# Optimization experiments

Measured on AMD Instinct MI355X. Metric: run time of the kernel, lower is better.

## Reference

```python
import jax, jax.numpy as jnp
import numpy as np

B, S, D_IN, D_EMB, H = 2, 2048, 1024, 1024, 16
HD = D_EMB // H  # projection_dim = 64


def setup_inputs() -> dict:
    key = jax.random.key(0)
    ks = jax.random.split(key, 9)
    s_in = 1.0 / np.sqrt(D_IN)
    s_emb = 1.0 / np.sqrt(D_EMB)
    return {
        "inputs": jax.random.normal(ks[0], (B, S, D_IN), dtype=jnp.float32),
        "Wq": jax.random.uniform(ks[1], (D_IN, D_EMB), jnp.float32, -s_in, s_in),
        "bq": jax.random.uniform(ks[2], (D_EMB,), jnp.float32, -s_in, s_in),
        "Wk": jax.random.uniform(ks[3], (D_IN, D_EMB), jnp.float32, -s_in, s_in),
        "bk": jax.random.uniform(ks[4], (D_EMB,), jnp.float32, -s_in, s_in),
        "Wv": jax.random.uniform(ks[5], (D_IN, D_EMB), jnp.float32, -s_in, s_in),
        "bv": jax.random.uniform(ks[6], (D_EMB,), jnp.float32, -s_in, s_in),
        "Wo": jax.random.uniform(ks[7], (D_EMB, D_EMB), jnp.float32, -s_emb, s_emb),
        "bo": jax.random.uniform(ks[8], (D_EMB,), jnp.float32, -s_emb, s_emb),
    }


def reference(inputs, Wq, bq, Wk, bk, Wv, bv, Wo, bo):
    b, s, _ = inputs.shape
    # QKV projections -> [b, h, s, hd]
    def split_heads(x):
        return x.reshape(b, s, H, HD).transpose(0, 2, 1, 3)
    q = split_heads(inputs @ Wq + bq)
    k = split_heads(inputs @ Wk + bk)
    v = split_heads(inputs @ Wv + bv)
    scale = 1.0 / jnp.sqrt(jnp.float32(HD))
    logits = jnp.einsum('bhqd,bhkd->bhqk', q, k) * scale
    attn = jax.nn.softmax(logits, axis=-1)
    ctx = jnp.einsum('bhqk,bhkd->bhqd', attn, v)  # [b,h,s,hd]
    concat = ctx.transpose(0, 2, 1, 3).reshape(b, s, D_EMB)
    return concat @ Wo + bo
```

## Files before the change

### kernel.cpp

```cpp
#include <hip/hip_runtime.h>
#include <stdint.h>

#define S_ 2048
#define H_ 16

typedef short s16x8 __attribute__((ext_vector_type(8)));
typedef float f32x4 __attribute__((ext_vector_type(4)));
typedef float f32x16 __attribute__((ext_vector_type(16)));

__device__ __forceinline__ ushort f2bf(float f) {
    union { float f; uint32_t u; } v; v.f = f;
    uint32_t r = v.u + 0x7fffu + ((v.u >> 16) & 1u);
    return (ushort)(r >> 16);
}
__device__ __forceinline__ uint32_t cvtpk(float a, float b) {
    uint32_t r;
    asm("v_cvt_pk_bf16_f32 %0, %1, %2" : "=v"(r) : "v"(a), "v"(b));
    return r;
}
__device__ __forceinline__ void plswap(uint32_t& a, uint32_t& b) {
    auto r = __builtin_amdgcn_permlane32_swap((int)a, (int)b, false, false);
    a = (uint32_t)r[0];
    b = (uint32_t)r[1];
}
__device__ __forceinline__ float xmax32(float x) {
    uint32_t a = __float_as_uint(x), b = a;
    plswap(a, b);
    return fmaxf(__uint_as_float(a), __uint_as_float(b));
}
__device__ __forceinline__ float xadd32(float x) {
    uint32_t a = __float_as_uint(x), b = a;
    plswap(a, b);
    return __uint_as_float(a) + __uint_as_float(b);
}
__device__ __forceinline__ float exp2_fast(float x) {
    float r;
    asm("v_exp_f32 %0, %1" : "=v"(r) : "v"(x));
    return r;
}

__device__ __forceinline__ void gld16(ushort* lds, const ushort* g) {
    auto* gp = reinterpret_cast<uint32_t __attribute__((address_space(1)))*>(
        reinterpret_cast<uintptr_t>(g));
    auto* lp = reinterpret_cast<uint32_t __attribute__((address_space(3)))*>(
        reinterpret_cast<uintptr_t>(lds));
    __builtin_amdgcn_global_load_lds(gp, lp, 16, 0, 0);
}

__global__ void cast_bf16(const float* __restrict__ src, ushort* __restrict__ dst) {
    size_t i = ((size_t)blockIdx.x * 256 + threadIdx.x) * 8;
    float4 x = *(const float4*)(src + i);
    float4 y = *(const float4*)(src + i + 4);
    s16x8 r;
    r[0] = (short)f2bf(x.x); r[1] = (short)f2bf(x.y);
    r[2] = (short)f2bf(x.z); r[3] = (short)f2bf(x.w);
    r[4] = (short)f2bf(y.x); r[5] = (short)f2bf(y.y);
    r[6] = (short)f2bf(y.z); r[7] = (short)f2bf(y.w);
    *(s16x8*)(dst + i) = r;
}

__global__ void transpose_k4(const float* __restrict__ s0, const float* __restrict__ s1,
                             const float* __restrict__ s2, const float* __restrict__ s3,
                             ushort* __restrict__ d0, ushort* __restrict__ d1,
                             ushort* __restrict__ d2, ushort* __restrict__ d3) {
    const int z = blockIdx.z;
    const float* src = (z == 0) ? s0 : (z == 1) ? s1 : (z == 2) ? s2 : s3;
    ushort* dst      = (z == 0) ? d0 : (z == 1) ? d1 : (z == 2) ? d2 : d3;
    __shared__ ushort t[32][33];
    int bx = blockIdx.x * 32, by = blockIdx.y * 32;
    int x = threadIdx.x;
    for (int y = threadIdx.y; y < 32; y += 8)
        t[y][x] = f2bf(src[(size_t)(by + y) * 1024 + bx + x]);
    __syncthreads();
    for (int y = threadIdx.y; y < 32; y += 8)
        dst[(size_t)(bx + y) * 1024 + by + x] = t[x][y];
}

__global__ void gemm_bt(const ushort* __restrict__ A,
                        const ushort* __restrict__ Bt0, const ushort* __restrict__ Bt1,
                        const ushort* __restrict__ Bt2,
                        const float* __restrict__ bi0, const float* __restrict__ bi1,
                        const float* __restrict__ bi2,
                        void* __restrict__ o0, void* __restrict__ o1,
                        void* __restrict__ o2,
                        int mode0) {
    const int z = blockIdx.z;
    const ushort* Bt  = (z == 0) ? Bt0 : (z == 1) ? Bt1 : Bt2;
    const float* bia  = (z == 0) ? bi0 : (z == 1) ? bi1 : bi2;
    void* out         = (z == 0) ? o0  : (z == 1) ? o1  : o2;
    const int mode = mode0 + z;

    __shared__ __align__(16) ushort SMEM[2][4096];
    ushort* Asm = &SMEM[0][0];
    ushort* Bsm = &SMEM[1][0];

    const int t = threadIdx.x;
    const int lane = t & 63, w = t >> 6;
    const int wm = w >> 1, wn = w & 1;
    const int quad = lane >> 4, l16 = lane & 15;
    const int m0 = blockIdx.y * 128, n0 = blockIdx.x * 128;
    const int K = 1024;

    const f32x4 FZ = {0.f, 0.f, 0.f, 0.f};
    f32x4 acc[4][4];
#pragma unroll
    for (int i = 0; i < 4; i++)
#pragma unroll
        for (int j = 0; j < 4; j++) acc[i][j] = FZ;

    const ushort* Ap = A  + (size_t)(m0 + (t >> 2)) * K + (t & 3) * 8;
    const ushort* Bp = Bt + (size_t)(n0 + (t >> 2)) * K + (t & 3) * 8;
    ushort* AsmW = Asm + w * 512;
    ushort* BsmW = Bsm + w * 512;

    for (int kt = 0; kt < K / 32; ++kt) {
        __syncthreads();
        gld16(AsmW,        Ap + kt * 32);
        gld16(AsmW + 2048, Ap + (size_t)64 * K + kt * 32);
        gld16(BsmW,        Bp + kt * 32);
        gld16(BsmW + 2048, Bp + (size_t)64 * K + kt * 32);
        __syncthreads();

        s16x8 a[4], b[4];
#pragma unroll
        for (int i = 0; i < 4; i++) {
            int row = wm * 64 + i * 16 + l16;
            a[i] = *(const s16x8*)((const char*)Asm + row * 64 + quad * 16);
        }
#pragma unroll
        for (int j = 0; j < 4; j++) {
            int row = wn * 64 + j * 16 + l16;
            b[j] = *(const s16x8*)((const char*)Bsm + row * 64 + quad * 16);
        }
#pragma unroll
        for (int i = 0; i < 4; i++)
#pragma unroll
            for (int j = 0; j < 4; j++)
                acc[i][j] = __builtin_amdgcn_mfma_f32_16x16x32_bf16(a[i], b[j], acc[i][j], 0, 0, 0);
    }

    if (mode == 3) {
        ushort* T = Asm;
        const int b_ = m0 >> 11;
        const int s_base = m0 & 2047;
        __syncthreads();
#pragma unroll
        for (int half = 0; half < 2; ++half) {
            if (wn == half) {
#pragma unroll
                for (int j = 0; j < 4; j++) {
                    int nl = j * 16 + l16;
                    float bv = bia[n0 + half * 64 + nl];
#pragma unroll
                    for (int i = 0; i < 4; i++) {
#pragma unroll
                        for (int r = 0; r < 4; r++) {
                            int ml = wm * 64 + i * 16 + quad * 4 + r;
                            T[nl * 128 + (ml ^ ((nl & 15) << 3))] = f2bf(acc[i][j][r] + bv);
                        }
                    }
                }
            }
            __syncthreads();
            {
                int row = t >> 2, cg = (t & 3) * 32;
                int ng = n0 + half * 64 + row;
                int h = ng >> 6, d = ng & 63;
                ushort* op = (ushort*)out + ((size_t)((b_ * 16 + h) * 64 + d)) * 2048 + s_base + cg;
#pragma unroll
                for (int c = 0; c < 4; c++) {
                    int col = (cg + c * 8) ^ ((row & 15) << 3);
                    *(s16x8*)(op + c * 8) = *(const s16x8*)(T + row * 128 + col);
                }
            }
            __syncthreads();
        }
        return;
    }

#pragma unroll
    for (int j = 0; j < 4; j++) {
        int n = n0 + wn * 64 + j * 16 + l16;
        float bv = bia[n];
#pragma unroll
        for (int i = 0; i < 4; i++) {
#pragma unroll
            for (int r = 0; r < 4; r++) {
                int m = m0 + wm * 64 + i * 16 + quad * 4 + r;
                float v = acc[i][j][r] + bv;
                if (mode == 0) {
                    ((float*)out)[(size_t)m * 1024 + n] = v;
                } else {
                    int b_ = m >> 11, s = m & 2047;
                    int h = n >> 6, d = n & 63;
                    if (mode == 1)
                        ((ushort*)out)[((size_t)(b_ * 16 + h) * 2048 + s) * 64 + d] = f2bf(v * 0.18033688011112042f);
                    else
                        ((ushort*)out)[((size_t)(b_ * 16 + h) * 2048 + s) * 64 + d] = f2bf(v);
                }
            }
        }
    }
}

#define MFMA32(a, b, c) __builtin_amdgcn_mfma_f32_32x32x16_bf16(a, b, c, 0, 0, 0)

__global__ __launch_bounds__(256, 2) void attn(const ushort* __restrict__ q_ws,
                                               const ushort* __restrict__ k_ws,
                                               const ushort* __restrict__ vt_ws,
                                               ushort* __restrict__ ctx) {
    __shared__ __align__(16) ushort Kb[2][4096];
    __shared__ __align__(16) ushort Vb[2][4096];
    __shared__ ushort obuf[4][32][72];

    const int t = threadIdx.x, lane = t & 63, w = t >> 6;
    const int l32 = lane & 31, hi = lane >> 5;

    const int bid = blockIdx.x;
    const int j_ = bid >> 3;
    const int bh = (bid & 7) + 8 * (j_ >> 4);
    const int q0 = (j_ & 15) * 128 + w * 32;

    const ushort* Qg = q_ws + (size_t)bh * S_ * 64;
    const ushort* Kg = k_ws + (size_t)bh * S_ * 64;
    const ushort* Vg = vt_ws + (size_t)bh * 64 * S_;

    s16x8 qf[4];
#pragma unroll
    for (int dc = 0; dc < 4; dc++)
        qf[dc] = *(const s16x8*)&Qg[(size_t)(q0 + l32) * 64 + dc * 16 + hi * 8];

    const int sr = t >> 3;
    const int sc = (t & 7) ^ (sr & 7);
    const ushort* kS = Kg + sr * 64 + sc * 8;
    const ushort* vS = Vg + (size_t)sr * 2048 + sc * 8;
    ushort* ldsK0 = &Kb[0][w * 512];
    ushort* ldsV0 = &Vb[0][w * 512];
    ushort* ldsK1 = &Kb[1][w * 512];
    ushort* ldsV1 = &Vb[1][w * 512];

    int fo[4];
#pragma unroll
    for (int c = 0; c < 4; c++)
        fo[c] = l32 * 64 + ((((c << 1) | hi) ^ (l32 & 7)) << 3);

    const f32x16 Z16 = {0.f,0.f,0.f,0.f,0.f,0.f,0.f,0.f,0.f,0.f,0.f,0.f,0.f,0.f,0.f,0.f};
    f32x16 o0 = Z16, o1 = Z16;
    float m_run = -1e30f, l_run = 0.f;

    gld16(ldsK0,        kS);
    gld16(ldsK0 + 2048, kS + 2048);
    gld16(ldsV0,        vS);
    gld16(ldsV0 + 2048, vS + (size_t)32 * 2048);
    __syncthreads();

    for (int kt = 0; kt < S_ / 64; ++kt) {
        const int cur = kt & 1;
        if (kt != S_ / 64 - 1) {
            const ushort* kn = kS + (kt + 1) * 4096;
            const ushort* vn = vS + (kt + 1) * 64;
            ushort* dK = cur ? ldsK0 : ldsK1;
            ushort* dV = cur ? ldsV0 : ldsV1;
            gld16(dK,        kn);
            gld16(dK + 2048, kn + 2048);
            gld16(dV,        vn);
            gld16(dV + 2048, vn + (size_t)32 * 2048);
        }
        const ushort* KB = &Kb[cur][0];
        const ushort* VB = &Vb[cur][0];

        f32x16 s0 = Z16, s1 = Z16;
#pragma unroll
        for (int dc = 0; dc < 4; dc++) {
            s16x8 k0 = *(const s16x8*)(KB + fo[dc]);
            s16x8 k1 = *(const s16x8*)(KB + 2048 + fo[dc]);
            s0 = MFMA32(k0, qf[dc], s0);
            s1 = MFMA32(k1, qf[dc], s1);
        }

        float m0 = fmaxf(s0[0], s1[0]), m1 = fmaxf(s0[1], s1[1]);
        float m2 = fmaxf(s0[2], s1[2]), m3 = fmaxf(s0[3], s1[3]);
#pragma unroll
        for (int r = 4; r < 16; r += 4) {
            m0 = fmaxf(m0, fmaxf(s0[r],     s1[r]));
            m1 = fmaxf(m1, fmaxf(s0[r + 1], s1[r + 1]));
            m2 = fmaxf(m2, fmaxf(s0[r + 2], s1[r + 2]));
            m3 = fmaxf(m3, fmaxf(s0[r + 3], s1[r + 3]));
        }
        float mx = fmaxf(fmaxf(m0, m1), fmaxf(m2, m3));
        mx = xmax32(mx);
        float mnew = fmaxf(m_run, mx);
        float alpha = exp2_fast(m_run - mnew);
        m_run = mnew;

        float ra = 0.f, rb = 0.f;
#pragma unroll
        for (int r = 0; r < 16; r++) {
            s0[r] = exp2_fast(s0[r] - mnew); ra += s0[r];
            s1[r] = exp2_fast(s1[r] - mnew); rb += s1[r];
        }
        l_run = l_run * alpha + xadd32(ra + rb);

#pragma unroll
        for (int r = 0; r < 16; r++) { o0[r] *= alpha; o1[r] *= alpha; }

#pragma unroll
        for (int ks = 0; ks < 2; ks++) {
            const f32x16& p = ks ? s1 : s0;
            uint32_t u0 = cvtpk(p[0], p[1]),   u2 = cvtpk(p[4], p[5]);
            plswap(u0, u2);
            uint32_t u1 = cvtpk(p[2], p[3]),   u3 = cvtpk(p[6], p[7]);
            plswap(u1, u3);
            uint32_t w0 = cvtpk(p[8], p[9]),   w2 = cvtpk(p[12], p[13]);
            plswap(w0, w2);
            uint32_t w1 = cvtpk(p[10], p[11]), w3 = cvtpk(p[14], p[15]);
            plswap(w1, w3);
            union { uint32_t u[4]; s16x8 h; } F0, F1;
            F0.u[0] = u0; F0.u[1] = u1; F0.u[2] = u2; F0.u[3] = u3;
            F1.u[0] = w0; F1.u[1] = w1; F1.u[2] = w2; F1.u[3] = w3;

            const int kc0 = ks * 2, kc1 = ks * 2 + 1;
            s16x8 v00 = *(const s16x8*)(VB + fo[kc0]);
            s16x8 v01 = *(const s16x8*)(VB + 2048 + fo[kc0]);
            s16x8 v10 = *(const s16x8*)(VB + fo[kc1]);
            s16x8 v11 = *(const s16x8*)(VB + 2048 + fo[kc1]);
            o0 = MFMA32(v00, F0.h, o0); o1 = MFMA32(v01, F0.h, o1);
            o0 = MFMA32(v10, F1.h, o0); o1 = MFMA32(v11, F1.h, o1);
        }

        __syncthreads();
    }

    float inv = 1.0f / l_run;
#pragma unroll
    for (int r = 0; r < 16; r++) {
        int d0 = (r & 3) + 8 * (r >> 2) + 4 * hi;
        obuf[w][l32][d0]      = f2bf(o0[r] * inv);
        obuf[w][l32][32 + d0] = f2bf(o1[r] * inv);
    }
    asm volatile("s_waitcnt lgkmcnt(0)" ::: "memory");
    __builtin_amdgcn_sched_barrier(0);
    int b_ = bh >> 4, h = bh & 15;
    ushort* gp = ctx + ((size_t)(b_ * 2048 + q0 + l32)) * 1024 + h * 64 + hi * 32;
#pragma unroll
    for (int c = 0; c < 4; c++)
        *(s16x8*)(gp + c * 8) = *(const s16x8*)&obuf[w][l32][hi * 32 + c * 8];
}

extern "C" void kernel_launch(void* const* d_in, const int* in_sizes, int n_in,
                              void* d_out, int out_size, void* d_ws, size_t ws_size,
                              hipStream_t stream) {
    const float* X  = (const float*)d_in[0];
    const float* Wq = (const float*)d_in[1];
    const float* bq = (const float*)d_in[2];
    const float* Wk = (const float*)d_in[3];
    const float* bk = (const float*)d_in[4];
    const float* Wv = (const float*)d_in[5];
    const float* bv = (const float*)d_in[6];
    const float* Wo = (const float*)d_in[7];
    const float* bo = (const float*)d_in[8];
    float* out = (float*)d_out;

    char* ws = (char*)d_ws;
    ushort* wtq  = (ushort*)(ws);
    ushort* wtk  = (ushort*)(ws + ((size_t)2 << 20));
    ushort* wtv  = (ushort*)(ws + ((size_t)4 << 20));
    ushort* wto  = (ushort*)(ws + ((size_t)6 << 20));
    ushort* qws  = (ushort*)(ws + ((size_t)8 << 20));
    ushort* kws  = (ushort*)(ws + ((size_t)16 << 20));
    ushort* ctx  = (ushort*)(ws + ((size_t)24 << 20));
    ushort* vtws = (ushort*)d_out;
    ushort* xbf  = (ushort*)d_out + ((size_t)4 << 20);

    transpose_k4<<<dim3(32, 32, 4), dim3(32, 8), 0, stream>>>(Wq, Wk, Wv, Wo,
                                                              wtq, wtk, wtv, wto);
    cast_bf16<<<2048, 256, 0, stream>>>(X, xbf);

    gemm_bt<<<dim3(8, 32, 3), 256, 0, stream>>>(xbf, wtq, wtk, wtv, bq, bk, bv,
                                                qws, kws, vtws, 1);

    attn<<<dim3(512), 256, 0, stream>>>(qws, kws, vtws, ctx);

    gemm_bt<<<dim3(8, 32, 1), 256, 0, stream>>>(ctx, wto, wto, wto, bo, bo, bo,
                                                out, out, out, 0);
}
```

Before: 207.7 us.

## Use 256x256 double-buffered GEMM tiles and lazy softmax rescaling in attention

The projection GEMMs move from 128x128 tiles with a 32-wide K step to 256x256 tiles with 512 threads, a 64-wide K step, XOR-swizzled LDS and double-buffered global-to-LDS staging, plus barrier and priority hints around the MFMA bursts. The attention kernel now rescales its running max, sum and output accumulators only when some lane's new max exceeds the old one by more than 8, which cuts the per-tile exp and multiply work. Larger tiles give more reuse per load, but the grid becomes small (64 blocks for the output projection, 192 for QKV), which may underfill the GPU's CUs. Letting the max lag by up to 8 in log2 space relies on the fp32 accumulators having enough headroom to avoid overflow.

Measured after the change: 215.2 us. 1.04x slower.

```diff
diff --git a/kernel.cpp b/kernel.cpp
--- a/kernel.cpp
+++ b/kernel.cpp
@@ -76,101 +76,132 @@
         dst[(size_t)(bx + y) * 1024 + by + x] = t[x][y];
 }
 
-__global__ void gemm_bt(const ushort* __restrict__ A,
-                        const ushort* __restrict__ Bt0, const ushort* __restrict__ Bt1,
-                        const ushort* __restrict__ Bt2,
-                        const float* __restrict__ bi0, const float* __restrict__ bi1,
-                        const float* __restrict__ bi2,
-                        void* __restrict__ o0, void* __restrict__ o1,
-                        void* __restrict__ o2,
-                        int mode0) {
+#define MFMA16(a, b, c) __builtin_amdgcn_mfma_f32_16x16x32_bf16(a, b, c, 0, 0, 0)
+
+__global__ __launch_bounds__(512, 2) void gemm256(
+        const ushort* __restrict__ A,
+        const ushort* __restrict__ Bt0, const ushort* __restrict__ Bt1,
+        const ushort* __restrict__ Bt2,
+        const float* __restrict__ bi0, const float* __restrict__ bi1,
+        const float* __restrict__ bi2,
+        void* __restrict__ o0, void* __restrict__ o1, void* __restrict__ o2,
+        int mode0) {
     const int z = blockIdx.z;
     const ushort* Bt  = (z == 0) ? Bt0 : (z == 1) ? Bt1 : Bt2;
     const float* bia  = (z == 0) ? bi0 : (z == 1) ? bi1 : bi2;
     void* out         = (z == 0) ? o0  : (z == 1) ? o1  : o2;
     const int mode = mode0 + z;
 
-    __shared__ __align__(16) ushort SMEM[2][4096];
-    ushort* Asm = &SMEM[0][0];
-    ushort* Bsm = &SMEM[1][0];
+    __shared__ __align__(16) ushort LB[2][2][16384];
 
     const int t = threadIdx.x;
     const int lane = t & 63, w = t >> 6;
-    const int wm = w >> 1, wn = w & 1;
+    const int wm = w >> 2, wn = w & 3;
     const int quad = lane >> 4, l16 = lane & 15;
-    const int m0 = blockIdx.y * 128, n0 = blockIdx.x * 128;
+    const int m0 = blockIdx.y * 256, n0 = blockIdx.x * 256;
     const int K = 1024;
+    const int NTK = K / 64;
 
     const f32x4 FZ = {0.f, 0.f, 0.f, 0.f};
-    f32x4 acc[4][4];
-#pragma unroll
-    for (int i = 0; i < 4; i++)
+    f32x4 acc[8][4];
+#pragma unroll
+    for (int i = 0; i < 8; i++)
 #pragma unroll
         for (int j = 0; j < 4; j++) acc[i][j] = FZ;
 
-    const ushort* Ap = A  + (size_t)(m0 + (t >> 2)) * K + (t & 3) * 8;
-    const ushort* Bp = Bt + (size_t)(n0 + (t >> 2)) * K + (t & 3) * 8;
-    ushort* AsmW = Asm + w * 512;
-    ushort* BsmW = Bsm + w * 512;
-
-    for (int kt = 0; kt < K / 32; ++kt) {
+    const int rr = t >> 3;
+    const int ck = (((t & 7) ^ (rr & 7)) * 8);
+    const ushort* sA0 = A  + (size_t)(m0 + rr) * K + ck;
+    const ushort* sB0 = Bt + (size_t)(n0 + rr) * K + ck;
+    const int wbase = w * 64 * 8;
+
+#define STAGE(buf, kt) do {                                              \
+    const int _o = (kt) * 64;                                            \
+    gld16(&LB[buf][0][wbase],            sA0 + _o);                      \
+    gld16(&LB[buf][0][wbase + 4096],     sA0 + (size_t)64  * K + _o);    \
+    gld16(&LB[buf][0][wbase + 8192],     sA0 + (size_t)128 * K + _o);    \
+    gld16(&LB[buf][0][wbase + 12288],    sA0 + (size_t)192 * K + _o);    \
+    gld16(&LB[buf][1][wbase],            sB0 + _o);                      \
+    gld16(&LB[buf][1][wbase + 4096],     sB0 + (size_t)64  * K + _o);    \
+    gld16(&LB[buf][1][wbase + 8192],     sB0 + (size_t)128 * K + _o);    \
+    gld16(&LB[buf][1][wbase + 12288],    sB0 + (size_t)192 * K + _o);    \
+} while (0)
+
+    const int fx = l16 & 7;
+    const int ckA0 = ((0 + quad) ^ fx) * 8;
+    const int ckA1 = ((4 + quad) ^ fx) * 8;
+    const int aOff = (wm * 128 + l16) * 64;
+    const int bOff = (wn * 64 + l16) * 64;
+
+    STAGE(0, 0);
+    __syncthreads();
+
+    for (int kt = 0; kt < NTK; ++kt) {
+        const int cur = kt & 1;
+        if (kt + 1 < NTK) STAGE(cur ^ 1, kt + 1);
+        const ushort* Ab = &LB[cur][0][0];
+        const ushort* Bb = &LB[cur][1][0];
+
+        s16x8 bf[4][2];
+#pragma unroll
+        for (int j = 0; j < 4; j++) {
+            bf[j][0] = *(const s16x8*)&Bb[bOff + j * 1024 + ckA0];
+            bf[j][1] = *(const s16x8*)&Bb[bOff + j * 1024 + ckA1];
+        }
+#pragma unroll
+        for (int p = 0; p < 4; ++p) {
+            s16x8 af[2][2];
+#pragma unroll
+            for (int i2 = 0; i2 < 2; i2++) {
+                af[i2][0] = *(const s16x8*)&Ab[aOff + (p * 2 + i2) * 1024 + ckA0];
+                af[i2][1] = *(const s16x8*)&Ab[aOff + (p * 2 + i2) * 1024 + ckA1];
+            }
+            __builtin_amdgcn_s_barrier();
+            __builtin_amdgcn_s_setprio(1);
+#pragma unroll
+            for (int i2 = 0; i2 < 2; i2++)
+#pragma unroll
+                for (int j = 0; j < 4; j++) {
+                    acc[p * 2 + i2][j] = MFMA16(af[i2][0], bf[j][0], acc[p * 2 + i2][j]);
+                    acc[p * 2 + i2][j] = MFMA16(af[i2][1], bf[j][1], acc[p * 2 + i2][j]);
+                }
+            __builtin_amdgcn_s_setprio(0);
+        }
         __syncthreads();
-        gld16(AsmW,        Ap + kt * 32);
-        gld16(AsmW + 2048, Ap + (size_t)64 * K + kt * 32);
-        gld16(BsmW,        Bp + kt * 32);
-        gld16(BsmW + 2048, Bp + (size_t)64 * K + kt * 32);
+    }
+
+    if (mode == 3) {
+        ushort* T = &LB[0][0][0];
+        const int b_ = m0 >> 11, s_base = m0 & 2047;
         __syncthreads();
-
-        s16x8 a[4], b[4];
-#pragma unroll
-        for (int i = 0; i < 4; i++) {
-            int row = wm * 64 + i * 16 + l16;
-            a[i] = *(const s16x8*)((const char*)Asm + row * 64 + quad * 16);
-        }
-#pragma unroll
-        for (int j = 0; j < 4; j++) {
-            int row = wn * 64 + j * 16 + l16;
-            b[j] = *(const s16x8*)((const char*)Bsm + row * 64 + quad * 16);
-        }
-#pragma unroll
-        for (int i = 0; i < 4; i++)
-#pragma unroll
-            for (int j = 0; j < 4; j++)
-                acc[i][j] = __builtin_amdgcn_mfma_f32_16x16x32_bf16(a[i], b[j], acc[i][j], 0, 0, 0);
-    }
-
-    if (mode == 3) {
-        ushort* T = Asm;
-        const int b_ = m0 >> 11;
-        const int s_base = m0 & 2047;
-        __syncthreads();
-#pragma unroll
-        for (int half = 0; half < 2; ++half) {
-            if (wn == half) {
+#pragma unroll
+        for (int pass = 0; pass < 4; ++pass) {
+            if (wn == pass) {
 #pragma unroll
                 for (int j = 0; j < 4; j++) {
                     int nl = j * 16 + l16;
-                    float bv = bia[n0 + half * 64 + nl];
-#pragma unroll
-                    for (int i = 0; i < 4; i++) {
+                    float bv = bia[n0 + pass * 64 + nl];
+#pragma unroll
+                    for (int i = 0; i < 8; i++) {
 #pragma unroll
                         for (int r = 0; r < 4; r++) {
-                            int ml = wm * 64 + i * 16 + quad * 4 + r;
-                            T[nl * 128 + (ml ^ ((nl & 15) << 3))] = f2bf(acc[i][j][r] + bv);
+                            int ml = wm * 128 + i * 16 + quad * 4 + r;
+                            T[nl * 256 + (ml ^ ((nl & 15) << 3))] = f2bf(acc[i][j][r] + bv);
                         }
                     }
                 }
             }
             __syncthreads();
             {
-                int row = t >> 2, cg = (t & 3) * 32;
-                int ng = n0 + half * 64 + row;
+                int row = t >> 3, cb = (t & 7) * 4;
+                int ng = n0 + pass * 64 + row;
                 int h = ng >> 6, d = ng & 63;
-                ushort* op = (ushort*)out + ((size_t)((b_ * 16 + h) * 64 + d)) * 2048 + s_base + cg;
+                ushort* op = (ushort*)out + ((size_t)((b_ * 16 + h) * 64 + d)) * 2048
+                             + s_base + (t & 7) * 32;
 #pragma unroll
                 for (int c = 0; c < 4; c++) {
-                    int col = (cg + c * 8) ^ ((row & 15) << 3);
-                    *(s16x8*)(op + c * 8) = *(const s16x8*)(T + row * 128 + col);
+                    int cc = (cb + c) ^ (row & 15);
+                    *(s16x8*)(op + c * 8) = *(const s16x8*)&T[row * 256 + cc * 8];
                 }
             }
             __syncthreads();
@@ -183,10 +214,10 @@
         int n = n0 + wn * 64 + j * 16 + l16;
         float bv = bia[n];
 #pragma unroll
-        for (int i = 0; i < 4; i++) {
+        for (int i = 0; i < 8; i++) {
 #pragma unroll
             for (int r = 0; r < 4; r++) {
-                int m = m0 + wm * 64 + i * 16 + quad * 4 + r;
+                int m = m0 + wm * 128 + i * 16 + quad * 4 + r;
                 float v = acc[i][j][r] + bv;
                 if (mode == 0) {
                     ((float*)out)[(size_t)m * 1024 + n] = v;
@@ -201,6 +232,7 @@
             }
         }
     }
+#undef STAGE
 }
 
 #define MFMA32(a, b, c) __builtin_amdgcn_mfma_f32_32x32x16_bf16(a, b, c, 0, 0, 0)
@@ -289,20 +321,23 @@
         }
         float mx = fmaxf(fmaxf(m0, m1), fmaxf(m2, m3));
         mx = xmax32(mx);
-        float mnew = fmaxf(m_run, mx);
-        float alpha = exp2_fast(m_run - mnew);
-        m_run = mnew;
+
+        if (__any(mx > m_run + 8.f)) {
+            float mnew = fmaxf(m_run, mx);
+            float alpha = exp2_fast(m_run - mnew);
+            m_run = mnew;
+            l_run *= alpha;
+#pragma unroll
+            for (int r = 0; r < 16; r++) { o0[r] *= alpha; o1[r] *= alpha; }
+        }
 
         float ra = 0.f, rb = 0.f;
 #pragma unroll
         for (int r = 0; r < 16; r++) {
-            s0[r] = exp2_fast(s0[r] - mnew); ra += s0[r];
-            s1[r] = exp2_fast(s1[r] - mnew); rb += s1[r];
-        }
-        l_run = l_run * alpha + xadd32(ra + rb);
-
-#pragma unroll
-        for (int r = 0; r < 16; r++) { o0[r] *= alpha; o1[r] *= alpha; }
+            s0[r] = exp2_fast(s0[r] - m_run); ra += s0[r];
+            s1[r] = exp2_fast(s1[r] - m_run); rb += s1[r];
+        }
+        l_run += xadd32(ra + rb);
 
 #pragma unroll
         for (int ks = 0; ks < 2; ks++) {
@@ -376,11 +411,11 @@
                                                               wtq, wtk, wtv, wto);
     cast_bf16<<<2048, 256, 0, stream>>>(X, xbf);
 
-    gemm_bt<<<dim3(8, 32, 3), 256, 0, stream>>>(xbf, wtq, wtk, wtv, bq, bk, bv,
+    gemm256<<<dim3(4, 16, 3), 512, 0, stream>>>(xbf, wtq, wtk, wtv, bq, bk, bv,
                                                 qws, kws, vtws, 1);
 
     attn<<<dim3(512), 256, 0, stream>>>(qws, kws, vtws, ctx);
 
-    gemm_bt<<<dim3(8, 32, 1), 256, 0, stream>>>(ctx, wto, wto, wto, bo, bo, bo,
+    gemm256<<<dim3(4, 16, 1), 512, 0, stream>>>(ctx, wto, wto, wto, bo, bo, bo,
                                                 out, out, out, 0);
 }
```
